# Kernel tuning notes

Hardware: AMD Instinct MI355X
Metric: run time of the kernel (lower is better)

The kernel has to match this reference:

```python
import jax, jax.numpy as jnp
import numpy as np

D = 1024   # d_model
HS = 64    # head_size
H = D // HS
B, T = 4, 2048
EPS = 1e-5


def setup_inputs() -> dict:
    key = jax.random.key(0)
    ks = jax.random.split(key, 8)
    s = 1.0 / np.sqrt(D)
    mk = lambda k: (jax.random.normal(k, (D, D), jnp.float32) * s)
    return {
        "x": jax.random.normal(ks[0], (B, T, D), jnp.float32),
        "ln_g": jnp.ones((D,), jnp.float32),
        "ln_b": jnp.zeros((D,), jnp.float32),
        "Wx": mk(ks[1]),
        "Ww": mk(ks[2]),
        "bw": jnp.zeros((D,), jnp.float32),
        "Wk": mk(ks[3]),
        "Wv": mk(ks[4]),
        "Wr": mk(ks[5]),
        "Wo": mk(ks[6]),
    }


def reference(x, ln_g, ln_b, Wx, Ww, bw, Wk, Wv, Wr, Wo):
    Bb, Tt, C = x.shape
    nh, hs = C // HS, HS
    # LayerNorm (population variance, matching torch nn.LayerNorm)
    mu = x.mean(-1, keepdims=True)
    var = x.var(-1, keepdims=True)
    xn = (x - mu) / jnp.sqrt(var + EPS) * ln_g + ln_b
    # projections (weights stored pre-transposed: y = x @ W)
    w = jax.nn.sigmoid((xn @ Wx) @ Ww + bw).reshape(Bb, Tt, nh, hs)
    k = (xn @ Wk).reshape(Bb, Tt, nh, hs)
    v = (xn @ Wv).reshape(Bb, Tt, nh, hs)
    r = jax.nn.sigmoid(xn @ Wr).reshape(Bb, Tt, nh, hs)

    def step(state, inp):
        kt, vt, wt, rt = inp  # each [B, H, hs]
        # outer product kv [B,H,hs,hs]; row-wise decay by (1 - w_t)
        state = (1.0 - wt)[..., None] * state + kt[..., None] * vt[..., None, :]
        out = jnp.einsum('bhd,bhde->bhe', rt, state)
        return state, out

    init = jnp.zeros((Bb, nh, hs, hs), x.dtype)
    tm = lambda a: jnp.moveaxis(a, 1, 0)  # time-major for scan
    state, outs = jax.lax.scan(step, init, (tm(k), tm(v), tm(w), tm(r)))
    y = jnp.moveaxis(outs, 0, 1).reshape(Bb, Tt, C) @ Wo
    return (y, state)
```

## Files before the change

### kernel.cpp

```cpp
#include <hip/hip_runtime.h>

#define ROWS 8192
#define DD   1024
#define TT   2048
#define NH   16
#define HS   64
#define CH   32
#define NC   (TT / CH)

typedef __attribute__((ext_vector_type(8))) short short8;
typedef __attribute__((ext_vector_type(4))) float f32x4;
typedef __attribute__((ext_vector_type(4))) unsigned short us4;
typedef unsigned short u16;

__device__ __forceinline__ u16 f2bf(float f) {
  unsigned u = __builtin_bit_cast(unsigned, f);
  u += 0x7fffu + ((u >> 16) & 1u);
  return (u16)(u >> 16);
}

__device__ __forceinline__ float bf2f(u16 h) {
  return __builtin_bit_cast(float, (unsigned)h << 16);
}

__device__ __forceinline__ void gload16(const void* g, void* l) {
  __builtin_amdgcn_global_load_lds(
      (const __attribute__((address_space(1))) unsigned int*)g,
      (__attribute__((address_space(3))) unsigned int*)l, 16, 0, 0);
}

__global__ __launch_bounds__(256) void transpose_cast(const float* __restrict__ W,
                                                      u16* __restrict__ WT) {
  __shared__ float tile[32][33];
  const int tx = threadIdx.x, ty = threadIdx.y;
  const int bx = blockIdx.x, by = blockIdx.y;
#pragma unroll
  for (int j = 0; j < 4; ++j)
    tile[ty + j * 8][tx] = W[(size_t)(by * 32 + ty + j * 8) * DD + bx * 32 + tx];
  __syncthreads();
#pragma unroll
  for (int j = 0; j < 4; ++j)
    WT[(size_t)(bx * 32 + ty + j * 8) * DD + by * 32 + tx] = f2bf(tile[tx][ty + j * 8]);
}

__global__ __launch_bounds__(256) void ln_kernel(const float* __restrict__ x,
                                                 const float* __restrict__ g,
                                                 const float* __restrict__ b,
                                                 u16* __restrict__ xn) {
  const int row = blockIdx.x;
  const int tid = threadIdx.x;
  const float4 v = reinterpret_cast<const float4*>(x + (size_t)row * DD)[tid];
  float s = v.x + v.y + v.z + v.w;
  float s2 = v.x * v.x + v.y * v.y + v.z * v.z + v.w * v.w;
#pragma unroll
  for (int o = 32; o > 0; o >>= 1) { s += __shfl_down(s, o); s2 += __shfl_down(s2, o); }
  __shared__ float red[8];
  const int wv = tid >> 6;
  if ((tid & 63) == 0) { red[wv] = s; red[4 + wv] = s2; }
  __syncthreads();
  s = red[0] + red[1] + red[2] + red[3];
  s2 = red[4] + red[5] + red[6] + red[7];
  const float mu = s * (1.f / 1024.f);
  const float var = s2 * (1.f / 1024.f) - mu * mu;
  const float rstd = rsqrtf(var + 1e-5f);
  const float4 gg = reinterpret_cast<const float4*>(g)[tid];
  const float4 bb = reinterpret_cast<const float4*>(b)[tid];
  us4 o4;
  o4.x = f2bf((v.x - mu) * rstd * gg.x + bb.x);
  o4.y = f2bf((v.y - mu) * rstd * gg.y + bb.y);
  o4.z = f2bf((v.z - mu) * rstd * gg.z + bb.z);
  o4.w = f2bf((v.w - mu) * rstd * gg.w + bb.w);
  *reinterpret_cast<us4*>(xn + (size_t)row * DD + tid * 4) = o4;
}

template <int EPI>
__global__ __launch_bounds__(256) void gemm_bt(const u16* __restrict__ A,
                                               const u16* __restrict__ BT,
                                               float* __restrict__ Cf,
                                               u16* __restrict__ Cb,
                                               const float* __restrict__ bias,
                                               int M, int N, int K) {
  __shared__ u16 lA[2][128 * 32];
  __shared__ u16 lB[2][128 * 32];
  const int tid = threadIdx.x;
  const int bx = blockIdx.x, by = blockIdx.y;
  const int lane = tid & 63, wid = tid >> 6;
  const int wr = wid >> 1, wc = wid & 1;
  const int sr = tid >> 2, sc = (tid & 3) * 8;
  const u16* gA = A + (size_t)(by * 128 + sr) * K + sc;
  const u16* gB = BT + (size_t)(bx * 128 + sr) * K + sc;

  f32x4 acc[4][4];
#pragma unroll
  for (int m = 0; m < 4; ++m)
#pragma unroll
    for (int n = 0; n < 4; ++n) acc[m][n] = (f32x4){0.f, 0.f, 0.f, 0.f};

  auto stage = [&](int buf, int kt) {
    const u16* a0 = gA + kt * 32;
    const u16* b0 = gB + kt * 32;
    gload16(a0, &lA[buf][tid * 8]);
    gload16(a0 + (size_t)64 * K, &lA[buf][2048 + tid * 8]);
    gload16(b0, &lB[buf][tid * 8]);
    gload16(b0 + (size_t)64 * K, &lB[buf][2048 + tid * 8]);
  };

  stage(0, 0);
  const int fr = lane & 15, fk = (lane >> 4) * 8;
  int cur = 0;
  const int nk = K / 32;
  for (int kt = 0; kt < nk; ++kt) {
    __syncthreads();
    if (kt + 1 < nk) stage(cur ^ 1, kt + 1);
    short8 af[4], bv[4];
#pragma unroll
    for (int m = 0; m < 4; ++m)
      af[m] = *reinterpret_cast<const short8*>(&lA[cur][(wr * 64 + m * 16 + fr) * 32 + fk]);
#pragma unroll
    for (int n = 0; n < 4; ++n)
      bv[n] = *reinterpret_cast<const short8*>(&lB[cur][(wc * 64 + n * 16 + fr) * 32 + fk]);
#pragma unroll
    for (int m = 0; m < 4; ++m)
#pragma unroll
      for (int n = 0; n < 4; ++n)
        acc[m][n] = __builtin_amdgcn_mfma_f32_16x16x32_bf16(af[m], bv[n], acc[m][n], 0, 0, 0);
    cur ^= 1;
  }

  const int er = (lane >> 4) * 4, ec = lane & 15;
#pragma unroll
  for (int m = 0; m < 4; ++m) {
    const int row0 = by * 128 + wr * 64 + m * 16 + er;
#pragma unroll
    for (int n = 0; n < 4; ++n) {
      const int col = bx * 128 + wc * 64 + n * 16 + ec;
#pragma unroll
      for (int i = 0; i < 4; ++i) {
        const float val = acc[m][n][i];
        const size_t idx = (size_t)(row0 + i) * N + col;
        if constexpr (EPI == 0) {
          Cb[idx] = f2bf(val);
        } else if constexpr (EPI == 1) {
          Cf[idx] = val;
        } else if constexpr (EPI == 2) {
          Cf[idx] = 1.f / (1.f + __expf(-val));
        } else {
          const float z = val + bias[col];
          Cf[idx] = 1.f / (1.f + __expf(z));
        }
      }
    }
  }
}

__global__ __launch_bounds__(256) void scan_phase1(const float* __restrict__ omw,
                                                   const float* __restrict__ kk,
                                                   const float* __restrict__ vv,
                                                   u16* __restrict__ U,
                                                   float* __restrict__ P) {
  __shared__ float win[2 * 3072];
  const int c = blockIdx.x, bh = blockIdx.y;
  const int tid = threadIdx.x;
  const int lane = tid & 63;
  const int wid = tid >> 6;
  const int dbase = __builtin_amdgcn_readfirstlane(wid << 4);
  const size_t chainBase = (size_t)(bh >> 4) * TT * DD + (size_t)(bh & 15) * HS;
  const size_t base0 = chainBase + (size_t)c * CH * DD;

  auto stage = [&](int buf, int w2) {
#pragma unroll
    for (int j = 0; j < 3; ++j) {
      const int idx = tid + 256 * j;
      const int a = idx >> 8, rem = idx & 255, tt = rem >> 4, f4c = rem & 15;
      const float* s = (a == 0) ? omw : (a == 1) ? kk : vv;
      gload16(s + base0 + (size_t)(w2 * 16 + tt) * DD + f4c * 4,
              &win[buf * 3072 + idx * 4]);
    }
  };

  float st[16];
#pragma unroll
  for (int i = 0; i < 16; ++i) st[i] = 0.f;
  const int pd = dbase + (lane & 15);
  float vp = 1.f;

  stage(0, 0);
  __syncthreads();
  int buf = 0;
  for (int w2 = 0; w2 < CH / 16; ++w2) {
    if (w2 + 1 < CH / 16) stage(buf ^ 1, w2 + 1);
    const float* wb = &win[buf * 3072];
#pragma unroll
    for (int tt = 0; tt < 16; ++tt) {
      const float4* o4 = (const float4*)&wb[       tt * 64 + dbase];
      const float4* k4 = (const float4*)&wb[1024 + tt * 64 + dbase];
      const float ve  = wb[2048 + tt * 64 + lane];
      vp *= wb[tt * 64 + pd];
#pragma unroll
      for (int i4 = 0; i4 < 4; ++i4) {
        const float4 o = o4[i4], k = k4[i4];
        st[4*i4+0] = __builtin_fmaf(o.x, st[4*i4+0], k.x * ve);
        st[4*i4+1] = __builtin_fmaf(o.y, st[4*i4+1], k.y * ve);
        st[4*i4+2] = __builtin_fmaf(o.z, st[4*i4+2], k.z * ve);
        st[4*i4+3] = __builtin_fmaf(o.w, st[4*i4+3], k.w * ve);
      }
    }
    __syncthreads();
    buf ^= 1;
  }
  u16* __restrict__ Ub = U + ((size_t)c * 64 + bh) * 4096;
#pragma unroll
  for (int i = 0; i < 16; ++i) Ub[(dbase + i) * 64 + lane] = f2bf(st[i]);
  if (lane < 16) P[((size_t)c * 64 + bh) * 64 + dbase + lane] = vp;
}

__global__ __launch_bounds__(256) void scan_phase2(u16* __restrict__ U,
                                                   const float* __restrict__ P,
                                                   float* __restrict__ stateOut) {
  const int bh = blockIdx.x;
  const int ds = blockIdx.y;
  const int tid = threadIdx.x;
  const int d = ds * 4 + (tid >> 6);
  const int e = tid & 63;
  const size_t el = (size_t)d * 64 + e;

  float S = 0.f;
  size_t ub = (size_t)bh * 4096 + el;
  size_t pb = (size_t)bh * 64 + d;
  u16 u_c = U[ub];
  float p_c = P[pb];
  for (int c = 0; c < NC; ++c) {
    u16 u_n = u_c; float p_n = p_c;
    if (c + 1 < NC) {
      u_n = U[ub + (size_t)64 * 4096];
      p_n = P[pb + (size_t)64 * 64];
    }
    U[ub] = f2bf(S);
    S = __builtin_fmaf(p_c, S, bf2f(u_c));
    u_c = u_n; p_c = p_n;
    ub += (size_t)64 * 4096;
    pb += (size_t)64 * 64;
  }
  stateOut[(size_t)bh * 4096 + el] = S;
}

__global__ __launch_bounds__(256) void scan_phase3(const float* __restrict__ omw,
                                                   const float* __restrict__ kk,
                                                   const float* __restrict__ vv,
                                                   const float* __restrict__ rr,
                                                   const u16* __restrict__ S_start,
                                                   u16* __restrict__ outs) {
  __shared__ float win[2 * 4096];
  __shared__ float part[4][16][64];
  const int c = blockIdx.x, bh = blockIdx.y;
  const int tid = threadIdx.x;
  const int lane = tid & 63;
  const int wid = tid >> 6;
  const int dbase = __builtin_amdgcn_readfirstlane(wid << 4);
  const size_t chainBase = (size_t)(bh >> 4) * TT * DD + (size_t)(bh & 15) * HS;
  const size_t base0 = chainBase + (size_t)c * CH * DD;

  auto stage = [&](int buf, int w2) {
#pragma unroll
    for (int j = 0; j < 4; ++j) {
      const int idx = tid + 256 * j;
      const int a = idx >> 8, rem = idx & 255, tt = rem >> 4, f4c = rem & 15;
      const float* s = (a == 0) ? omw : (a == 1) ? kk : (a == 2) ? rr : vv;
      gload16(s + base0 + (size_t)(w2 * 16 + tt) * DD + f4c * 4,
              &win[buf * 4096 + idx * 4]);
    }
  };

  float st[16];
  const u16* __restrict__ Sb = S_start + ((size_t)c * 64 + bh) * 4096;
#pragma unroll
  for (int i = 0; i < 16; ++i) st[i] = bf2f(Sb[(dbase + i) * 64 + lane]);

  stage(0, 0);
  __syncthreads();
  int buf = 0;
  for (int w2 = 0; w2 < CH / 16; ++w2) {
    if (w2 + 1 < CH / 16) stage(buf ^ 1, w2 + 1);
    const float* wb = &win[buf * 4096];
#pragma unroll
    for (int tt = 0; tt < 16; ++tt) {
      const float4* o4 = (const float4*)&wb[       tt * 64 + dbase];
      const float4* k4 = (const float4*)&wb[1024 + tt * 64 + dbase];
      const float4* r4 = (const float4*)&wb[2048 + tt * 64 + dbase];
      const float ve  = wb[3072 + tt * 64 + lane];
      float a0 = 0.f, a1 = 0.f;
#pragma unroll
      for (int i4 = 0; i4 < 4; ++i4) {
        const float4 o = o4[i4], k = k4[i4], r = r4[i4];
        st[4*i4+0] = __builtin_fmaf(o.x, st[4*i4+0], k.x * ve);
        a0 = __builtin_fmaf(r.x, st[4*i4+0], a0);
        st[4*i4+1] = __builtin_fmaf(o.y, st[4*i4+1], k.y * ve);
        a1 = __builtin_fmaf(r.y, st[4*i4+1], a1);
        st[4*i4+2] = __builtin_fmaf(o.z, st[4*i4+2], k.z * ve);
        a0 = __builtin_fmaf(r.z, st[4*i4+2], a0);
        st[4*i4+3] = __builtin_fmaf(o.w, st[4*i4+3], k.w * ve);
        a1 = __builtin_fmaf(r.w, st[4*i4+3], a1);
      }
      part[wid][tt][lane] = a0 + a1;
    }
    __syncthreads();
#pragma unroll
    for (int s = 0; s < 4; ++s) {
      const int tt = wid * 4 + s;
      const float sum = (part[0][tt][lane] + part[1][tt][lane]) +
                        (part[2][tt][lane] + part[3][tt][lane]);
      outs[base0 + (size_t)(w2 * 16 + tt) * DD + lane] = f2bf(sum);
    }
    __syncthreads();
    buf ^= 1;
  }
}

extern "C" void kernel_launch(void* const* d_in, const int* in_sizes, int n_in,
                              void* d_out, int out_size, void* d_ws, size_t ws_size,
                              hipStream_t stream) {
  const float* x   = (const float*)d_in[0];
  const float* lng = (const float*)d_in[1];
  const float* lnb = (const float*)d_in[2];
  const float* Wx  = (const float*)d_in[3];
  const float* Ww  = (const float*)d_in[4];
  const float* bw  = (const float*)d_in[5];
  const float* Wk  = (const float*)d_in[6];
  const float* Wv  = (const float*)d_in[7];
  const float* Wr  = (const float*)d_in[8];
  const float* Wo  = (const float*)d_in[9];
  float* out = (float*)d_out;
  char* ws = (char*)d_ws;

  const size_t SZ_W = (size_t)DD * DD * 2;
  u16* WxT = (u16*)(ws + 0 * SZ_W);
  u16* WwT = (u16*)(ws + 1 * SZ_W);
  u16* WkT = (u16*)(ws + 2 * SZ_W);
  u16* WvT = (u16*)(ws + 3 * SZ_W);
  u16* WrT = (u16*)(ws + 4 * SZ_W);
  u16* WoT = (u16*)(ws + 5 * SZ_W);
  size_t off = 6 * SZ_W;
  const size_t SZ_ABF = (size_t)ROWS * DD * 2;
  u16* xn   = (u16*)(ws + off); off += SZ_ABF;
  u16* pbuf = (u16*)(ws + off); off += SZ_ABF;
  u16* outs = (u16*)(ws + off); off += SZ_ABF;
  const size_t SZ_AF = (size_t)ROWS * DD * 4;
  float* omw = (float*)(ws + off); off += SZ_AF;
  float* kf  = (float*)(ws + off); off += SZ_AF;
  float* vf  = (float*)(ws + off); off += SZ_AF;
  float* rf  = (float*)(ws + off); off += SZ_AF;
  u16*   Ubuf = xn;
  float* Pbuf = (float*)WxT;
  (void)ws_size; (void)in_sizes; (void)n_in; (void)out_size;

  dim3 tpb(32, 8), tgrid(32, 32);
  transpose_cast<<<tgrid, tpb, 0, stream>>>(Wx, WxT);
  transpose_cast<<<tgrid, tpb, 0, stream>>>(Ww, WwT);
  transpose_cast<<<tgrid, tpb, 0, stream>>>(Wk, WkT);
  transpose_cast<<<tgrid, tpb, 0, stream>>>(Wv, WvT);
  transpose_cast<<<tgrid, tpb, 0, stream>>>(Wr, WrT);
  transpose_cast<<<tgrid, tpb, 0, stream>>>(Wo, WoT);

  ln_kernel<<<ROWS, 256, 0, stream>>>(x, lng, lnb, xn);

  dim3 ggrid(DD / 128, ROWS / 128), gblk(256);
  gemm_bt<0><<<ggrid, gblk, 0, stream>>>(xn, WxT, nullptr, pbuf, nullptr, ROWS, DD, DD);
  gemm_bt<3><<<ggrid, gblk, 0, stream>>>(pbuf, WwT, omw, nullptr, bw, ROWS, DD, DD);
  gemm_bt<1><<<ggrid, gblk, 0, stream>>>(xn, WkT, kf, nullptr, nullptr, ROWS, DD, DD);
  gemm_bt<1><<<ggrid, gblk, 0, stream>>>(xn, WvT, vf, nullptr, nullptr, ROWS, DD, DD);
  gemm_bt<2><<<ggrid, gblk, 0, stream>>>(xn, WrT, rf, nullptr, nullptr, ROWS, DD, DD);

  dim3 sgrid(NC, 64);
  scan_phase1<<<sgrid, 256, 0, stream>>>(omw, kf, vf, Ubuf, Pbuf);
  dim3 p2grid(64, 16);
  scan_phase2<<<p2grid, 256, 0, stream>>>(Ubuf, Pbuf, out + (size_t)ROWS * DD);
  scan_phase3<<<sgrid, 256, 0, stream>>>(omw, kf, vf, rf, Ubuf, outs);

  gemm_bt<1><<<ggrid, gblk, 0, stream>>>(outs, WoT, out, nullptr, nullptr, ROWS, DD, DD);
}
```

Before: 473.2 us.

## Store projection outputs in bf16 and read bf16 in scan kernels

The four projection GEMMs (1-w, k, v, sigmoid r) now write bf16 instead of fp32. The scan phase 1 and phase 3 kernels stage bf16 tiles into shared memory and convert to fp32 in registers. The per-wave partial outputs in shared memory are also stored as bf16. This halves the global write and read traffic of these intermediates and the LDS footprint, at the cost of lower precision in the decay factors and scan inputs, which can compound over the recurrence.

```diff
diff --git a/kernel.cpp b/kernel.cpp
--- a/kernel.cpp
+++ b/kernel.cpp
@@ -143,22 +143,22 @@
         } else if constexpr (EPI == 1) {
           Cf[idx] = val;
         } else if constexpr (EPI == 2) {
-          Cf[idx] = 1.f / (1.f + __expf(-val));
+          Cb[idx] = f2bf(1.f / (1.f + __expf(-val)));
         } else {
           const float z = val + bias[col];
-          Cf[idx] = 1.f / (1.f + __expf(z));
+          Cb[idx] = f2bf(1.f / (1.f + __expf(z)));
         }
       }
     }
   }
 }
 
-__global__ __launch_bounds__(256) void scan_phase1(const float* __restrict__ omw,
-                                                   const float* __restrict__ kk,
-                                                   const float* __restrict__ vv,
+__global__ __launch_bounds__(256) void scan_phase1(const u16* __restrict__ omw,
+                                                   const u16* __restrict__ kk,
+                                                   const u16* __restrict__ vv,
                                                    u16* __restrict__ U,
                                                    float* __restrict__ P) {
-  __shared__ float win[2 * 3072];
+  __shared__ u16 win[2 * 3072];
   const int c = blockIdx.x, bh = blockIdx.y;
   const int tid = threadIdx.x;
   const int lane = tid & 63;
@@ -169,12 +169,14 @@
 
   auto stage = [&](int buf, int w2) {
 #pragma unroll
-    for (int j = 0; j < 3; ++j) {
+    for (int j = 0; j < 2; ++j) {
       const int idx = tid + 256 * j;
-      const int a = idx >> 8, rem = idx & 255, tt = rem >> 4, f4c = rem & 15;
-      const float* s = (a == 0) ? omw : (a == 1) ? kk : vv;
-      gload16(s + base0 + (size_t)(w2 * 16 + tt) * DD + f4c * 4,
-              &win[buf * 3072 + idx * 4]);
+      if (idx < 384) {
+        const int a = idx >> 7, rem = idx & 127, tt = rem >> 3, seg = rem & 7;
+        const u16* s = (a == 0) ? omw : (a == 1) ? kk : vv;
+        gload16(s + base0 + (size_t)(w2 * 16 + tt) * DD + seg * 8,
+                &win[buf * 3072 + idx * 8]);
+      }
     }
   };
 
@@ -189,20 +191,19 @@
   int buf = 0;
   for (int w2 = 0; w2 < CH / 16; ++w2) {
     if (w2 + 1 < CH / 16) stage(buf ^ 1, w2 + 1);
-    const float* wb = &win[buf * 3072];
+    const u16* wb = &win[buf * 3072];
 #pragma unroll
     for (int tt = 0; tt < 16; ++tt) {
-      const float4* o4 = (const float4*)&wb[       tt * 64 + dbase];
-      const float4* k4 = (const float4*)&wb[1024 + tt * 64 + dbase];
-      const float ve  = wb[2048 + tt * 64 + lane];
-      vp *= wb[tt * 64 + pd];
-#pragma unroll
-      for (int i4 = 0; i4 < 4; ++i4) {
-        const float4 o = o4[i4], k = k4[i4];
-        st[4*i4+0] = __builtin_fmaf(o.x, st[4*i4+0], k.x * ve);
-        st[4*i4+1] = __builtin_fmaf(o.y, st[4*i4+1], k.y * ve);
-        st[4*i4+2] = __builtin_fmaf(o.z, st[4*i4+2], k.z * ve);
-        st[4*i4+3] = __builtin_fmaf(o.w, st[4*i4+3], k.w * ve);
+      const short8 o8a = *(const short8*)&wb[       tt * 64 + dbase];
+      const short8 o8b = *(const short8*)&wb[       tt * 64 + dbase + 8];
+      const short8 k8a = *(const short8*)&wb[1024 + tt * 64 + dbase];
+      const short8 k8b = *(const short8*)&wb[1024 + tt * 64 + dbase + 8];
+      const float ve  = bf2f(wb[2048 + tt * 64 + lane]);
+      vp *= bf2f(wb[tt * 64 + pd]);
+#pragma unroll
+      for (int i = 0; i < 8; ++i) {
+        st[i]     = __builtin_fmaf(bf2f((u16)o8a[i]), st[i],     bf2f((u16)k8a[i]) * ve);
+        st[8 + i] = __builtin_fmaf(bf2f((u16)o8b[i]), st[8 + i], bf2f((u16)k8b[i]) * ve);
       }
     }
     __syncthreads();
@@ -244,14 +245,14 @@
   stateOut[(size_t)bh * 4096 + el] = S;
 }
 
-__global__ __launch_bounds__(256) void scan_phase3(const float* __restrict__ omw,
-                                                   const float* __restrict__ kk,
-                                                   const float* __restrict__ vv,
-                                                   const float* __restrict__ rr,
+__global__ __launch_bounds__(256) void scan_phase3(const u16* __restrict__ omw,
+                                                   const u16* __restrict__ kk,
+                                                   const u16* __restrict__ vv,
+                                                   const u16* __restrict__ rr,
                                                    const u16* __restrict__ S_start,
                                                    u16* __restrict__ outs) {
-  __shared__ float win[2 * 4096];
-  __shared__ float part[4][16][64];
+  __shared__ u16 win[2 * 4096];
+  __shared__ u16 part[4][16][64];
   const int c = blockIdx.x, bh = blockIdx.y;
   const int tid = threadIdx.x;
   const int lane = tid & 63;
@@ -262,12 +263,12 @@
 
   auto stage = [&](int buf, int w2) {
 #pragma unroll
-    for (int j = 0; j < 4; ++j) {
+    for (int j = 0; j < 2; ++j) {
       const int idx = tid + 256 * j;
-      const int a = idx >> 8, rem = idx & 255, tt = rem >> 4, f4c = rem & 15;
-      const float* s = (a == 0) ? omw : (a == 1) ? kk : (a == 2) ? rr : vv;
-      gload16(s + base0 + (size_t)(w2 * 16 + tt) * DD + f4c * 4,
-              &win[buf * 4096 + idx * 4]);
+      const int a = idx >> 7, rem = idx & 127, tt = rem >> 3, seg = rem & 7;
+      const u16* s = (a == 0) ? omw : (a == 1) ? kk : (a == 2) ? rr : vv;
+      gload16(s + base0 + (size_t)(w2 * 16 + tt) * DD + seg * 8,
+              &win[buf * 4096 + idx * 8]);
     }
   };
 
@@ -281,34 +282,32 @@
   int buf = 0;
   for (int w2 = 0; w2 < CH / 16; ++w2) {
     if (w2 + 1 < CH / 16) stage(buf ^ 1, w2 + 1);
-    const float* wb = &win[buf * 4096];
+    const u16* wb = &win[buf * 4096];
 #pragma unroll
     for (int tt = 0; tt < 16; ++tt) {
-      const float4* o4 = (const float4*)&wb[       tt * 64 + dbase];
-      const float4* k4 = (const float4*)&wb[1024 + tt * 64 + dbase];
-      const float4* r4 = (const float4*)&wb[2048 + tt * 64 + dbase];
-      const float ve  = wb[3072 + tt * 64 + lane];
+      const short8 o8a = *(const short8*)&wb[       tt * 64 + dbase];
+      const short8 o8b = *(const short8*)&wb[       tt * 64 + dbase + 8];
+      const short8 k8a = *(const short8*)&wb[1024 + tt * 64 + dbase];
+      const short8 k8b = *(const short8*)&wb[1024 + tt * 64 + dbase + 8];
+      const short8 r8a = *(const short8*)&wb[2048 + tt * 64 + dbase];
+      const short8 r8b = *(const short8*)&wb[2048 + tt * 64 + dbase + 8];
+      const float ve  = bf2f(wb[3072 + tt * 64 + lane]);
       float a0 = 0.f, a1 = 0.f;
 #pragma unroll
-      for (int i4 = 0; i4 < 4; ++i4) {
-        const float4 o = o4[i4], k = k4[i4], r = r4[i4];
-        st[4*i4+0] = __builtin_fmaf(o.x, st[4*i4+0], k.x * ve);
-        a0 = __builtin_fmaf(r.x, st[4*i4+0], a0);
-        st[4*i4+1] = __builtin_fmaf(o.y, st[4*i4+1], k.y * ve);
-        a1 = __builtin_fmaf(r.y, st[4*i4+1], a1);
-        st[4*i4+2] = __builtin_fmaf(o.z, st[4*i4+2], k.z * ve);
-        a0 = __builtin_fmaf(r.z, st[4*i4+2], a0);
-        st[4*i4+3] = __builtin_fmaf(o.w, st[4*i4+3], k.w * ve);
-        a1 = __builtin_fmaf(r.w, st[4*i4+3], a1);
+      for (int i = 0; i < 8; ++i) {
+        st[i]     = __builtin_fmaf(bf2f((u16)o8a[i]), st[i],     bf2f((u16)k8a[i]) * ve);
+        a0 = __builtin_fmaf(bf2f((u16)r8a[i]), st[i], a0);
+        st[8 + i] = __builtin_fmaf(bf2f((u16)o8b[i]), st[8 + i], bf2f((u16)k8b[i]) * ve);
+        a1 = __builtin_fmaf(bf2f((u16)r8b[i]), st[8 + i], a1);
       }
-      part[wid][tt][lane] = a0 + a1;
+      part[wid][tt][lane] = f2bf(a0 + a1);
     }
     __syncthreads();
 #pragma unroll
     for (int s = 0; s < 4; ++s) {
       const int tt = wid * 4 + s;
-      const float sum = (part[0][tt][lane] + part[1][tt][lane]) +
-                        (part[2][tt][lane] + part[3][tt][lane]);
+      const float sum = (bf2f(part[0][tt][lane]) + bf2f(part[1][tt][lane])) +
+                        (bf2f(part[2][tt][lane]) + bf2f(part[3][tt][lane]));
       outs[base0 + (size_t)(w2 * 16 + tt) * DD + lane] = f2bf(sum);
     }
     __syncthreads();
@@ -344,11 +343,10 @@
   u16* xn   = (u16*)(ws + off); off += SZ_ABF;
   u16* pbuf = (u16*)(ws + off); off += SZ_ABF;
   u16* outs = (u16*)(ws + off); off += SZ_ABF;
-  const size_t SZ_AF = (size_t)ROWS * DD * 4;
-  float* omw = (float*)(ws + off); off += SZ_AF;
-  float* kf  = (float*)(ws + off); off += SZ_AF;
-  float* vf  = (float*)(ws + off); off += SZ_AF;
-  float* rf  = (float*)(ws + off); off += SZ_AF;
+  u16* omw = (u16*)(ws + off); off += SZ_ABF;
+  u16* kf  = (u16*)(ws + off); off += SZ_ABF;
+  u16* vf  = (u16*)(ws + off); off += SZ_ABF;
+  u16* rf  = (u16*)(ws + off); off += SZ_ABF;
   u16*   Ubuf = xn;
   float* Pbuf = (float*)WxT;
   (void)ws_size; (void)in_sizes; (void)n_in; (void)out_size;
@@ -365,10 +363,10 @@
 
   dim3 ggrid(DD / 128, ROWS / 128), gblk(256);
   gemm_bt<0><<<ggrid, gblk, 0, stream>>>(xn, WxT, nullptr, pbuf, nullptr, ROWS, DD, DD);
-  gemm_bt<3><<<ggrid, gblk, 0, stream>>>(pbuf, WwT, omw, nullptr, bw, ROWS, DD, DD);
-  gemm_bt<1><<<ggrid, gblk, 0, stream>>>(xn, WkT, kf, nullptr, nullptr, ROWS, DD, DD);
-  gemm_bt<1><<<ggrid, gblk, 0, stream>>>(xn, WvT, vf, nullptr, nullptr, ROWS, DD, DD);
-  gemm_bt<2><<<ggrid, gblk, 0, stream>>>(xn, WrT, rf, nullptr, nullptr, ROWS, DD, DD);
+  gemm_bt<3><<<ggrid, gblk, 0, stream>>>(pbuf, WwT, nullptr, omw, bw, ROWS, DD, DD);
+  gemm_bt<0><<<ggrid, gblk, 0, stream>>>(xn, WkT, nullptr, kf, nullptr, ROWS, DD, DD);
+  gemm_bt<0><<<ggrid, gblk, 0, stream>>>(xn, WvT, nullptr, vf, nullptr, ROWS, DD, DD);
+  gemm_bt<2><<<ggrid, gblk, 0, stream>>>(xn, WrT, nullptr, rf, nullptr, ROWS, DD, DD);
 
   dim3 sgrid(NC, 64);
   scan_phase1<<<sgrid, 256, 0, stream>>>(omw, kf, vf, Ubuf, Pbuf);
```

Result: slower. 549.1 us (+16.0%).
